# Optimization experiments

Measured on AMD Instinct MI355X. Metric: run time of the kernel, lower is better.

## Reference

```python
import jax, jax.numpy as jnp
import numpy as np

IN_F, HID, OUT, NN = 64, 128, 64, 128
TOTAL = 4096  # 32 graphs * 128 nodes


def setup_inputs() -> dict:
    key = jax.random.key(0)
    ks = jax.random.split(key, 8)
    d_in = 1 + 2 * IN_F
    s1 = 1.0 / np.sqrt(d_in)
    s2 = 1.0 / np.sqrt(HID)
    return {
        "feat": jax.random.normal(ks[0], (TOTAL, IN_F), jnp.float32),
        "coordinate": jax.random.normal(ks[1], (TOTAL, 3), jnp.float32),
        "W1": jax.random.uniform(ks[2], (d_in, HID), jnp.float32, -s1, s1),
        "b1": jax.random.uniform(ks[3], (HID,), jnp.float32, -s1, s1),
        "W2": jax.random.uniform(ks[4], (HID, HID), jnp.float32, -s2, s2),
        "b2": jax.random.uniform(ks[5], (HID,), jnp.float32, -s2, s2),
        "W3": jax.random.uniform(ks[6], (HID, OUT), jnp.float32, -s2, s2),
        "b3": jax.random.uniform(ks[7], (OUT,), jnp.float32, -s2, s2),
        "num_nodes": NN,
    }


def reference(feat, coordinate, W1, b1, W2, b2, W3, b3, num_nodes):
    N = num_nodes
    B = feat.shape[0] // N
    h = feat.reshape(B, N, -1)        # [B,N,F]
    x = coordinate.reshape(B, N, -1)  # [B,N,3]
    # pairwise squared distance: [B,N,N,1]
    d2 = jnp.sum((x[:, None, :, :] - x[:, :, None, :]) ** 2, axis=-1, keepdims=True)
    F = h.shape[-1]
    # feat concat order matches torch: [h_j broadcast over dim1, h_i broadcast over dim2]
    hj = jnp.broadcast_to(h[:, None, :, :], (B, N, N, F))
    hi = jnp.broadcast_to(h[:, :, None, :], (B, N, N, F))
    z = jnp.concatenate([d2, hj, hi], axis=-1)  # [B,N,N,1+2F]
    z = jax.nn.silu(z @ W1 + b1)
    z = jax.nn.silu(z @ W2 + b2)
    z = z @ W3 + b3                   # [B,N,N,OUT]
    return jnp.sum(z, axis=(1, 2))    # [B,OUT]
```

## Files before the change

### kernel.cpp

```cpp
#include <hip/hip_runtime.h>
#include <hip/hip_bf16.h>

#define F_IN 64
#define HID 128
#define OUTF 64
#define NN 128
#define NB 32
#define TOTAL 4096

typedef short bf16x8 __attribute__((ext_vector_type(8)));
typedef float f32x4 __attribute__((ext_vector_type(4)));

static __device__ __forceinline__ short f2bf(float v) {
  __hip_bfloat16 h = __float2bfloat16(v);
  return __builtin_bit_cast(short, h);
}
static __device__ __forceinline__ float fast_silu(float v) {
  return v * __builtin_amdgcn_rcpf(1.f + __expf(-v));
}

__global__ __launch_bounds__(256) void uv_prep(
    const float* __restrict__ feat,
    const float* __restrict__ W1,
    const float* __restrict__ W2,
    const float* __restrict__ b1,
    float* __restrict__ uv,
    __hip_bfloat16* __restrict__ w2swz) {
  __shared__ __align__(16) char wcat[256 * 128];
  const int tid = threadIdx.x;

  {
    const int c = tid;
    const int cc = c & 127;
    const int rbase = (c < HID) ? 1 : 65;
#pragma unroll
    for (int p = 0; p < 8; ++p) {
      bf16x8 pk;
#pragma unroll
      for (int m = 0; m < 8; ++m)
        pk[m] = f2bf(W1[(rbase + p * 8 + m) * HID + cc]);
      *reinterpret_cast<bf16x8*>(wcat + c * 128 + ((p ^ (c & 7)) << 4)) = pk;
    }
  }
  if (blockIdx.x < 64) {
    const int e = blockIdx.x * 256 + tid;
    const int kk = e >> 7, cc2 = e & 127;
    const int byo = cc2 * 256 + (((kk >> 3) ^ (cc2 & 7)) << 4) + (kk & 7) * 2;
    *reinterpret_cast<__hip_bfloat16*>(reinterpret_cast<char*>(w2swz) + byo) =
        __float2bfloat16(W2[kk * HID + cc2]);
  }
  __syncthreads();

  const int wave = tid >> 6, lane = tid & 63;
  const int lr = lane & 15, kg = lane >> 4;
  const int r0 = blockIdx.x * 16;

  f32x4 acc[4];
#pragma unroll
  for (int ct = 0; ct < 4; ++ct) acc[ct] = {0.f, 0.f, 0.f, 0.f};

#pragma unroll
  for (int ks = 0; ks < 2; ++ks) {
    const float* fp = feat + (size_t)(r0 + lr) * F_IN + ks * 32 + kg * 8;
    const f32x4 fa = *reinterpret_cast<const f32x4*>(fp);
    const f32x4 fb = *reinterpret_cast<const f32x4*>(fp + 4);
    bf16x8 a;
#pragma unroll
    for (int m = 0; m < 4; ++m) {
      a[m] = f2bf(fa[m]);
      a[4 + m] = f2bf(fb[m]);
    }
    const int slot = ks * 4 + kg;
#pragma unroll
    for (int ct = 0; ct < 4; ++ct) {
      const int c = wave * 64 + ct * 16 + lr;
      const bf16x8 w = *reinterpret_cast<const bf16x8*>(
          wcat + c * 128 + ((slot ^ (c & 7)) << 4));
      acc[ct] = __builtin_amdgcn_mfma_f32_16x16x32_bf16(a, w, acc[ct], 0, 0, 0);
    }
  }
#pragma unroll
  for (int ct = 0; ct < 4; ++ct) {
    const int c = wave * 64 + ct * 16 + lr;
    const float badd = (c >= HID) ? b1[c - HID] : 0.f;
#pragma unroll
    for (int reg = 0; reg < 4; ++reg) {
      const int r = r0 + kg * 4 + reg;
      uv[(size_t)r * 256 + c] = acc[ct][reg] + badd;
    }
  }
}

__global__ __launch_bounds__(512) void sake_main(
    const float* __restrict__ coord,
    const float* __restrict__ W1,
    const float* __restrict__ b2,
    const float* __restrict__ uv,
    const __hip_bfloat16* __restrict__ w2swz,
    float* __restrict__ part) {
  __shared__ __align__(16) char w2lds[HID * 256];
  __shared__ float ssum[8][HID];

  const int tid = threadIdx.x;
  const int bid = (blockIdx.x & 7) * 512 + (blockIdx.x >> 3);
  const int b = bid >> 7;
  const int i = bid & 127;

#pragma unroll
  for (int p = 0; p < 4; ++p) {
    const int o = (tid + p * 512) * 16;
    *reinterpret_cast<int4*>(w2lds + o) =
        *reinterpret_cast<const int4*>(reinterpret_cast<const char*>(w2swz) + o);
  }

  const int wave = tid >> 6, lane = tid & 63;
  const int lr = lane & 15, kg = lane >> 4;
  const int j = wave * 16 + lr;

  const float* xj = coord + (size_t)(b * NN + j) * 3;
  const float* xi = coord + (size_t)(b * NN + i) * 3;
  const float dx = xj[0] - xi[0], dy = xj[1] - xi[1], dz = xj[2] - xi[2];
  const float d2j = dx * dx + dy * dy + dz * dz;

  f32x4 acc[8];
#pragma unroll
  for (int ct = 0; ct < 8; ++ct) {
    const float bb = b2[ct * 16 + lr];
    acc[ct] = {bb, bb, bb, bb};
  }

  const float* urow = uv + (size_t)(b * NN + j) * 256;
  const float* vrow = uv + (size_t)(b * NN + i) * 256 + HID;

  __syncthreads();

#pragma unroll
  for (int ks = 0; ks < 4; ++ks) {
    const int c0 = ks * 32 + kg * 8;
    const f32x4 ua = *reinterpret_cast<const f32x4*>(urow + c0);
    const f32x4 ub = *reinterpret_cast<const f32x4*>(urow + c0 + 4);
    const f32x4 va = *reinterpret_cast<const f32x4*>(vrow + c0);
    const f32x4 vb = *reinterpret_cast<const f32x4*>(vrow + c0 + 4);
    const f32x4 wa = *reinterpret_cast<const f32x4*>(W1 + c0);
    const f32x4 wb = *reinterpret_cast<const f32x4*>(W1 + c0 + 4);
    bf16x8 a;
#pragma unroll
    for (int m = 0; m < 4; ++m) {
      a[m] = f2bf(fast_silu(fmaf(d2j, wa[m], ua[m] + va[m])));
      a[4 + m] = f2bf(fast_silu(fmaf(d2j, wb[m], ub[m] + vb[m])));
    }
    const int slot = ks * 4 + kg;
    const int rbase = lr * 256 + ((slot ^ (lr & 7)) << 4);
#pragma unroll
    for (int ct = 0; ct < 8; ++ct) {
      const bf16x8 w = *reinterpret_cast<const bf16x8*>(w2lds + rbase + ct * 4096);
      acc[ct] = __builtin_amdgcn_mfma_f32_16x16x32_bf16(a, w, acc[ct], 0, 0, 0);
    }
  }

  float csum[8];
#pragma unroll
  for (int ct = 0; ct < 8; ++ct) {
    float s = fast_silu(acc[ct][0]) + fast_silu(acc[ct][1]) +
              fast_silu(acc[ct][2]) + fast_silu(acc[ct][3]);
    s += __shfl_xor(s, 16);
    s += __shfl_xor(s, 32);
    csum[ct] = s;
  }
  if (lane < 16) {
#pragma unroll
    for (int ct = 0; ct < 8; ++ct) ssum[wave][ct * 16 + lane] = csum[ct];
  }
  __syncthreads();
  if (tid < HID) {
    float s = 0.f;
#pragma unroll
    for (int w = 0; w < 8; ++w) s += ssum[w][tid];
    part[(size_t)bid * HID + tid] = s;
  }
}

__global__ void final_kernel(const float* __restrict__ part,
                             const float* __restrict__ W3,
                             const float* __restrict__ b3,
                             float* __restrict__ out) {
  __shared__ float s2[2][HID];
  __shared__ float s[HID];
  int b = blockIdx.x, t = threadIdx.x;
  int c = t & 127, half = t >> 7;
  float a = 0.f;
  for (int i = half * 64; i < half * 64 + 64; ++i)
    a += part[(size_t)(b * NN + i) * HID + c];
  s2[half][c] = a;
  __syncthreads();
  if (t < HID) s[t] = s2[0][t] + s2[1][t];
  __syncthreads();
  if (t < OUTF) {
    float o = 16384.f * b3[t];
    for (int c2 = 0; c2 < HID; ++c2) o += s[c2] * W3[c2 * OUTF + t];
    out[b * OUTF + t] = o;
  }
}

extern "C" void kernel_launch(void* const* d_in, const int* in_sizes, int n_in,
                              void* d_out, int out_size, void* d_ws, size_t ws_size,
                              hipStream_t stream) {
  const float* feat = (const float*)d_in[0];
  const float* coord = (const float*)d_in[1];
  const float* W1 = (const float*)d_in[2];
  const float* b1 = (const float*)d_in[3];
  const float* W2 = (const float*)d_in[4];
  const float* b2 = (const float*)d_in[5];
  const float* W3 = (const float*)d_in[6];
  const float* b3 = (const float*)d_in[7];
  float* out = (float*)d_out;

  char* ws = (char*)d_ws;
  __hip_bfloat16* w2swz = (__hip_bfloat16*)ws;
  float* uv = (float*)(ws + 64 * 1024);
  float* part = (float*)(ws + 64 * 1024 + 4096 * 1024);

  uv_prep<<<256, 256, 0, stream>>>(feat, W1, W2, b1, uv, w2swz);
  sake_main<<<TOTAL, 512, 0, stream>>>(coord, W1, b2, uv, w2swz, part);
  final_kernel<<<NB, 256, 0, stream>>>(part, W3, b3, out);
}
```

Measured before the change: 70.54 us.

## Process four i-rows per block and reuse W2 fragments across j-tiles

Each block of sake_main now handles four i nodes instead of one, with two waves per i each covering 64 j columns as four 16-row tiles. W2 fragments are loaded from LDS once per k-step into registers and reused across the four tiles. The per-block W2 LDS fill is also amortised over four times more work, since the grid drops from 4096 to 1024 blocks. The cost is a 32-entry accumulator array per thread, which raises register pressure, and launch bounds now request two blocks per CU. The final reduction kernel is adjusted to match the new partial-sum layout.

```diff
diff --git a/kernel.cpp b/kernel.cpp
--- a/kernel.cpp
+++ b/kernel.cpp
@@ -91,7 +91,7 @@
   }
 }
 
-__global__ __launch_bounds__(512) void sake_main(
+__global__ __launch_bounds__(512, 2) void sake_main(
     const float* __restrict__ coord,
     const float* __restrict__ W1,
     const float* __restrict__ b2,
@@ -102,9 +102,9 @@
   __shared__ float ssum[8][HID];
 
   const int tid = threadIdx.x;
-  const int bid = (blockIdx.x & 7) * 512 + (blockIdx.x >> 3);
-  const int b = bid >> 7;
-  const int i = bid & 127;
+  const int bid = (blockIdx.x & 7) * 128 + (blockIdx.x >> 3);
+  const int b = bid >> 5;
+  const int ig = bid & 31;
 
 #pragma unroll
   for (int p = 0; p < 4; ++p) {
@@ -115,54 +115,75 @@
 
   const int wave = tid >> 6, lane = tid & 63;
   const int lr = lane & 15, kg = lane >> 4;
-  const int j = wave * 16 + lr;
-
-  const float* xj = coord + (size_t)(b * NN + j) * 3;
+  const int i = ig * 4 + (wave >> 1);
+  const int j0 = (wave & 1) * 64;
+
   const float* xi = coord + (size_t)(b * NN + i) * 3;
-  const float dx = xj[0] - xi[0], dy = xj[1] - xi[1], dz = xj[2] - xi[2];
-  const float d2j = dx * dx + dy * dy + dz * dz;
-
-  f32x4 acc[8];
+  const float xix = xi[0], xiy = xi[1], xiz = xi[2];
+  float d2t[4];
+#pragma unroll
+  for (int t = 0; t < 4; ++t) {
+    const float* xj = coord + (size_t)(b * NN + j0 + t * 16 + lr) * 3;
+    const float dx = xj[0] - xix, dy = xj[1] - xiy, dz = xj[2] - xiz;
+    d2t[t] = dx * dx + dy * dy + dz * dz;
+  }
+
+  f32x4 acc[4][8];
 #pragma unroll
   for (int ct = 0; ct < 8; ++ct) {
     const float bb = b2[ct * 16 + lr];
-    acc[ct] = {bb, bb, bb, bb};
-  }
-
-  const float* urow = uv + (size_t)(b * NN + j) * 256;
-  const float* vrow = uv + (size_t)(b * NN + i) * 256 + HID;
+#pragma unroll
+    for (int t = 0; t < 4; ++t) acc[t][ct] = {bb, bb, bb, bb};
+  }
+
+  const float* vrow = uv + ((size_t)b * NN + i) * 256 + HID;
+  const float* urow0 = uv + ((size_t)b * NN + j0 + lr) * 256;
 
   __syncthreads();
 
 #pragma unroll
   for (int ks = 0; ks < 4; ++ks) {
     const int c0 = ks * 32 + kg * 8;
-    const f32x4 ua = *reinterpret_cast<const f32x4*>(urow + c0);
-    const f32x4 ub = *reinterpret_cast<const f32x4*>(urow + c0 + 4);
+    bf16x8 wf[8];
+    const int rbase = lr * 256 + ((((ks << 2) | kg) ^ (lr & 7)) << 4);
+#pragma unroll
+    for (int ct = 0; ct < 8; ++ct)
+      wf[ct] = *reinterpret_cast<const bf16x8*>(w2lds + rbase + ct * 4096);
+
     const f32x4 va = *reinterpret_cast<const f32x4*>(vrow + c0);
     const f32x4 vb = *reinterpret_cast<const f32x4*>(vrow + c0 + 4);
     const f32x4 wa = *reinterpret_cast<const f32x4*>(W1 + c0);
     const f32x4 wb = *reinterpret_cast<const f32x4*>(W1 + c0 + 4);
-    bf16x8 a;
-#pragma unroll
-    for (int m = 0; m < 4; ++m) {
-      a[m] = f2bf(fast_silu(fmaf(d2j, wa[m], ua[m] + va[m])));
-      a[4 + m] = f2bf(fast_silu(fmaf(d2j, wb[m], ub[m] + vb[m])));
-    }
-    const int slot = ks * 4 + kg;
-    const int rbase = lr * 256 + ((slot ^ (lr & 7)) << 4);
-#pragma unroll
-    for (int ct = 0; ct < 8; ++ct) {
-      const bf16x8 w = *reinterpret_cast<const bf16x8*>(w2lds + rbase + ct * 4096);
-      acc[ct] = __builtin_amdgcn_mfma_f32_16x16x32_bf16(a, w, acc[ct], 0, 0, 0);
+
+#pragma unroll
+    for (int t = 0; t < 4; ++t) {
+      const float* up = urow0 + t * 4096 + c0;
+      const f32x4 ua = *reinterpret_cast<const f32x4*>(up);
+      const f32x4 ub = *reinterpret_cast<const f32x4*>(up + 4);
+      bf16x8 a;
+#pragma unroll
+      for (int m = 0; m < 4; ++m) {
+        a[m] = f2bf(fast_silu(fmaf(d2t[t], wa[m], ua[m] + va[m])));
+        a[4 + m] = f2bf(fast_silu(fmaf(d2t[t], wb[m], ub[m] + vb[m])));
+      }
+#pragma unroll
+      for (int ct = 0; ct < 8; ++ct)
+        acc[t][ct] = __builtin_amdgcn_mfma_f32_16x16x32_bf16(a, wf[ct],
+                                                             acc[t][ct], 0, 0, 0);
     }
   }
 
   float csum[8];
 #pragma unroll
   for (int ct = 0; ct < 8; ++ct) {
-    float s = fast_silu(acc[ct][0]) + fast_silu(acc[ct][1]) +
-              fast_silu(acc[ct][2]) + fast_silu(acc[ct][3]);
+    float s = 0.f;
+#pragma unroll
+    for (int t = 0; t < 4; ++t)
+#pragma unroll
+      for (int reg = 0; reg < 4; ++reg) {
+        const float v = acc[t][ct][reg];
+        s = fmaf(v, __builtin_amdgcn_rcpf(1.f + __expf(-v)), s);
+      }
     s += __shfl_xor(s, 16);
     s += __shfl_xor(s, 32);
     csum[ct] = s;
@@ -189,8 +210,8 @@
   int b = blockIdx.x, t = threadIdx.x;
   int c = t & 127, half = t >> 7;
   float a = 0.f;
-  for (int i = half * 64; i < half * 64 + 64; ++i)
-    a += part[(size_t)(b * NN + i) * HID + c];
+  for (int g = half * 16; g < half * 16 + 16; ++g)
+    a += part[(size_t)(b * 32 + g) * HID + c];
   s2[half][c] = a;
   __syncthreads();
   if (t < HID) s[t] = s2[0][t] + s2[1][t];
@@ -221,6 +242,6 @@
   float* part = (float*)(ws + 64 * 1024 + 4096 * 1024);
 
   uv_prep<<<256, 256, 0, stream>>>(feat, W1, W2, b1, uv, w2swz);
-  sake_main<<<TOTAL, 512, 0, stream>>>(coord, W1, b2, uv, w2swz, part);
+  sake_main<<<1024, 512, 0, stream>>>(coord, W1, b2, uv, w2swz, part);
   final_kernel<<<NB, 256, 0, stream>>>(part, W3, b3, out);
 }
```

Result: faster. 68.82 us (-2.4%).

## Hold W2 in registers, one wave per node i, prescale SiLU by -log2e

Applied to the files above, without the earlier changes.

The main kernel is restructured so each wave handles one target node i and loops over j in chunks of 16. Half of the transposed W2 stays in registers for the whole loop and the other half is reloaded from global memory on each chunk, which removes the shared-memory staging and the block-wide sync. The weights, biases and u/v are prescaled by -log2(e) so SiLU uses a raw exp2 without extra multiplies, and final_kernel undoes the scale with -ln2. Register pressure rises and the per-chunk W2 reloads depend on cache hits; the swapped MFMA operand order also changes the reduction layout to a 16-lane shuffle.

```diff
diff --git a/kernel.cpp b/kernel.cpp
--- a/kernel.cpp
+++ b/kernel.cpp
@@ -8,6 +8,9 @@
 #define NB 32
 #define TOTAL 4096
 
+#define NEG_LOG2E (-1.4426950408889634f)
+#define NEG_LN2 (-0.6931471805599453f)
+
 typedef short bf16x8 __attribute__((ext_vector_type(8)));
 typedef float f32x4 __attribute__((ext_vector_type(4)));
 
@@ -15,8 +18,13 @@
   __hip_bfloat16 h = __float2bfloat16(v);
   return __builtin_bit_cast(short, h);
 }
-static __device__ __forceinline__ float fast_silu(float v) {
-  return v * __builtin_amdgcn_rcpf(1.f + __expf(-v));
+
+static __device__ __forceinline__ float fexp2(float x) {
+#if __has_builtin(__builtin_amdgcn_exp2f)
+  return __builtin_amdgcn_exp2f(x);
+#else
+  return exp2f(x);
+#endif
 }
 
 __global__ __launch_bounds__(256) void uv_prep(
@@ -24,11 +32,13 @@
     const float* __restrict__ W1,
     const float* __restrict__ W2,
     const float* __restrict__ b1,
-    float* __restrict__ uv,
-    __hip_bfloat16* __restrict__ w2swz) {
+    const float* __restrict__ b2,
+    float* __restrict__ uvp,
+    __hip_bfloat16* __restrict__ w2t,
+    float* __restrict__ w0p,
+    float* __restrict__ b2p) {
   __shared__ __align__(16) char wcat[256 * 128];
   const int tid = threadIdx.x;
-
   {
     const int c = tid;
     const int cc = c & 127;
@@ -45,9 +55,10 @@
   if (blockIdx.x < 64) {
     const int e = blockIdx.x * 256 + tid;
     const int kk = e >> 7, cc2 = e & 127;
-    const int byo = cc2 * 256 + (((kk >> 3) ^ (cc2 & 7)) << 4) + (kk & 7) * 2;
-    *reinterpret_cast<__hip_bfloat16*>(reinterpret_cast<char*>(w2swz) + byo) =
-        __float2bfloat16(W2[kk * HID + cc2]);
+    w2t[cc2 * HID + kk] = __float2bfloat16(W2[kk * HID + cc2]);
+  } else if (blockIdx.x == 64) {
+    if (tid < HID) w0p[tid] = NEG_LOG2E * W1[tid];
+    else b2p[tid - HID] = NEG_LOG2E * b2[tid - HID];
   }
   __syncthreads();
 
@@ -86,97 +97,128 @@
 #pragma unroll
     for (int reg = 0; reg < 4; ++reg) {
       const int r = r0 + kg * 4 + reg;
-      uv[(size_t)r * 256 + c] = acc[ct][reg] + badd;
-    }
-  }
-}
-
-__global__ __launch_bounds__(512) void sake_main(
+      uvp[(size_t)r * 256 + c] = NEG_LOG2E * (acc[ct][reg] + badd);
+    }
+  }
+}
+
+__global__ __launch_bounds__(256, 2) void sake_main(
     const float* __restrict__ coord,
-    const float* __restrict__ W1,
-    const float* __restrict__ b2,
-    const float* __restrict__ uv,
-    const __hip_bfloat16* __restrict__ w2swz,
+    const float* __restrict__ w0p,
+    const float* __restrict__ b2p,
+    const float* __restrict__ uvp,
+    const __hip_bfloat16* __restrict__ w2t,
     float* __restrict__ part) {
-  __shared__ __align__(16) char w2lds[HID * 256];
-  __shared__ float ssum[8][HID];
-
   const int tid = threadIdx.x;
-  const int bid = (blockIdx.x & 7) * 512 + (blockIdx.x >> 3);
-  const int b = bid >> 7;
-  const int i = bid & 127;
-
-#pragma unroll
-  for (int p = 0; p < 4; ++p) {
-    const int o = (tid + p * 512) * 16;
-    *reinterpret_cast<int4*>(w2lds + o) =
-        *reinterpret_cast<const int4*>(reinterpret_cast<const char*>(w2swz) + o);
-  }
-
   const int wave = tid >> 6, lane = tid & 63;
   const int lr = lane & 15, kg = lane >> 4;
-  const int j = wave * 16 + lr;
-
-  const float* xj = coord + (size_t)(b * NN + j) * 3;
+  const int bid = (blockIdx.x & 7) * 128 + (blockIdx.x >> 3);
+  const int gi = bid * 4 + wave;
+  const int b = gi >> 7, i = gi & 127;
+
+  const short* w2s = reinterpret_cast<const short*>(w2t);
+
+  bf16x8 w2f[4][4];
+#pragma unroll
+  for (int cht = 0; cht < 4; ++cht)
+#pragma unroll
+    for (int ks = 0; ks < 4; ++ks)
+      w2f[cht][ks] = *reinterpret_cast<const bf16x8*>(
+          w2s + (cht * 16 + lr) * HID + ks * 32 + kg * 8);
+
   const float* xi = coord + (size_t)(b * NN + i) * 3;
-  const float dx = xj[0] - xi[0], dy = xj[1] - xi[1], dz = xj[2] - xi[2];
-  const float d2j = dx * dx + dy * dy + dz * dz;
-
-  f32x4 acc[8];
-#pragma unroll
-  for (int ct = 0; ct < 8; ++ct) {
-    const float bb = b2[ct * 16 + lr];
-    acc[ct] = {bb, bb, bb, bb};
-  }
-
-  const float* urow = uv + (size_t)(b * NN + j) * 256;
-  const float* vrow = uv + (size_t)(b * NN + i) * 256 + HID;
-
-  __syncthreads();
-
-#pragma unroll
-  for (int ks = 0; ks < 4; ++ks) {
-    const int c0 = ks * 32 + kg * 8;
-    const f32x4 ua = *reinterpret_cast<const f32x4*>(urow + c0);
-    const f32x4 ub = *reinterpret_cast<const f32x4*>(urow + c0 + 4);
-    const f32x4 va = *reinterpret_cast<const f32x4*>(vrow + c0);
-    const f32x4 vb = *reinterpret_cast<const f32x4*>(vrow + c0 + 4);
-    const f32x4 wa = *reinterpret_cast<const f32x4*>(W1 + c0);
-    const f32x4 wb = *reinterpret_cast<const f32x4*>(W1 + c0 + 4);
-    bf16x8 a;
+  const float xix = xi[0], xiy = xi[1], xiz = xi[2];
+  const float* vrow = uvp + ((size_t)b * NN + i) * 256 + HID;
+  const float* ubase = uvp + (size_t)b * NN * 256;
+
+  f32x4 csum[8];
+#pragma unroll
+  for (int c = 0; c < 8; ++c) csum[c] = {0.f, 0.f, 0.f, 0.f};
+
+#pragma unroll 2
+  for (int ch = 0; ch < 8; ++ch) {
+    const int j = ch * 16 + lr;
+
+    bf16x8 wl[4][4];
+#pragma unroll
+    for (int c4 = 0; c4 < 4; ++c4)
+#pragma unroll
+      for (int ks = 0; ks < 4; ++ks)
+        wl[c4][ks] = *reinterpret_cast<const bf16x8*>(
+            w2s + ((4 + c4) * 16 + lr) * HID + ks * 32 + kg * 8);
+
+    const float* xj = coord + (size_t)(b * NN + j) * 3;
+    const float dx = xj[0] - xix, dy = xj[1] - xiy, dz = xj[2] - xiz;
+    const float d2 = dx * dx + dy * dy + dz * dz;
+
+    const float* urow = ubase + (size_t)j * 256;
+    bf16x8 zb[4];
+#pragma unroll
+    for (int ks = 0; ks < 4; ++ks) {
+      const int c0 = ks * 32 + kg * 8;
+      const f32x4 ua = *reinterpret_cast<const f32x4*>(urow + c0);
+      const f32x4 ub = *reinterpret_cast<const f32x4*>(urow + c0 + 4);
+      const f32x4 va = *reinterpret_cast<const f32x4*>(vrow + c0);
+      const f32x4 vb = *reinterpret_cast<const f32x4*>(vrow + c0 + 4);
+      const f32x4 wa = *reinterpret_cast<const f32x4*>(w0p + c0);
+      const f32x4 wb = *reinterpret_cast<const f32x4*>(w0p + c0 + 4);
+#pragma unroll
+      for (int m = 0; m < 4; ++m) {
+        const float z = fmaf(d2, wa[m], ua[m] + va[m]);
+        const float s = z * __builtin_amdgcn_rcpf(1.f + fexp2(z));
+        zb[ks][m] = f2bf(s);
+      }
+#pragma unroll
+      for (int m = 0; m < 4; ++m) {
+        const float z = fmaf(d2, wb[m], ub[m] + vb[m]);
+        const float s = z * __builtin_amdgcn_rcpf(1.f + fexp2(z));
+        zb[ks][4 + m] = f2bf(s);
+      }
+    }
+
+    f32x4 acc[8];
+#pragma unroll
+    for (int c = 0; c < 8; ++c)
+      acc[c] = *reinterpret_cast<const f32x4*>(b2p + c * 16 + kg * 4);
+
+#pragma unroll
+    for (int ks = 0; ks < 4; ++ks) {
+#pragma unroll
+      for (int c = 0; c < 4; ++c)
+        acc[c] = __builtin_amdgcn_mfma_f32_16x16x32_bf16(w2f[c][ks], zb[ks],
+                                                         acc[c], 0, 0, 0);
+#pragma unroll
+      for (int c = 0; c < 4; ++c)
+        acc[4 + c] = __builtin_amdgcn_mfma_f32_16x16x32_bf16(wl[c][ks], zb[ks],
+                                                             acc[4 + c], 0, 0, 0);
+    }
+
+#pragma unroll
+    for (int c = 0; c < 8; ++c)
+#pragma unroll
+      for (int m = 0; m < 4; ++m) {
+        const float z = acc[c][m];
+        const float y = __builtin_amdgcn_rcpf(1.f + fexp2(z));
+        csum[c][m] = fmaf(z, y, csum[c][m]);
+      }
+  }
+
+#pragma unroll
+  for (int c = 0; c < 8; ++c)
 #pragma unroll
     for (int m = 0; m < 4; ++m) {
-      a[m] = f2bf(fast_silu(fmaf(d2j, wa[m], ua[m] + va[m])));
-      a[4 + m] = f2bf(fast_silu(fmaf(d2j, wb[m], ub[m] + vb[m])));
-    }
-    const int slot = ks * 4 + kg;
-    const int rbase = lr * 256 + ((slot ^ (lr & 7)) << 4);
-#pragma unroll
-    for (int ct = 0; ct < 8; ++ct) {
-      const bf16x8 w = *reinterpret_cast<const bf16x8*>(w2lds + rbase + ct * 4096);
-      acc[ct] = __builtin_amdgcn_mfma_f32_16x16x32_bf16(a, w, acc[ct], 0, 0, 0);
-    }
-  }
-
-  float csum[8];
-#pragma unroll
-  for (int ct = 0; ct < 8; ++ct) {
-    float s = fast_silu(acc[ct][0]) + fast_silu(acc[ct][1]) +
-              fast_silu(acc[ct][2]) + fast_silu(acc[ct][3]);
-    s += __shfl_xor(s, 16);
-    s += __shfl_xor(s, 32);
-    csum[ct] = s;
-  }
-  if (lane < 16) {
-#pragma unroll
-    for (int ct = 0; ct < 8; ++ct) ssum[wave][ct * 16 + lane] = csum[ct];
-  }
-  __syncthreads();
-  if (tid < HID) {
-    float s = 0.f;
-#pragma unroll
-    for (int w = 0; w < 8; ++w) s += ssum[w][tid];
-    part[(size_t)bid * HID + tid] = s;
+      float s = csum[c][m];
+      s += __shfl_xor(s, 1);
+      s += __shfl_xor(s, 2);
+      s += __shfl_xor(s, 4);
+      s += __shfl_xor(s, 8);
+      csum[c][m] = s;
+    }
+  if (lr == 0) {
+    float* dst = part + (size_t)gi * HID;
+#pragma unroll
+    for (int c = 0; c < 8; ++c)
+      *reinterpret_cast<f32x4*>(dst + c * 16 + kg * 4) = csum[c];
   }
 }
 
@@ -189,11 +231,11 @@
   int b = blockIdx.x, t = threadIdx.x;
   int c = t & 127, half = t >> 7;
   float a = 0.f;
-  for (int i = half * 64; i < half * 64 + 64; ++i)
-    a += part[(size_t)(b * NN + i) * HID + c];
+  for (int g = half * 64; g < half * 64 + 64; ++g)
+    a += part[(size_t)(b * NN + g) * HID + c];
   s2[half][c] = a;
   __syncthreads();
-  if (t < HID) s[t] = s2[0][t] + s2[1][t];
+  if (t < HID) s[t] = (s2[0][t] + s2[1][t]) * NEG_LN2;
   __syncthreads();
   if (t < OUTF) {
     float o = 16384.f * b3[t];
@@ -216,11 +258,13 @@
   float* out = (float*)d_out;
 
   char* ws = (char*)d_ws;
-  __hip_bfloat16* w2swz = (__hip_bfloat16*)ws;
-  float* uv = (float*)(ws + 64 * 1024);
+  __hip_bfloat16* w2t = (__hip_bfloat16*)ws;
+  float* w0p = (float*)(ws + 32 * 1024);
+  float* b2p = (float*)(ws + 36 * 1024);
+  float* uvp = (float*)(ws + 64 * 1024);
   float* part = (float*)(ws + 64 * 1024 + 4096 * 1024);
 
-  uv_prep<<<256, 256, 0, stream>>>(feat, W1, W2, b1, uv, w2swz);
-  sake_main<<<TOTAL, 512, 0, stream>>>(coord, W1, b2, uv, w2swz, part);
+  uv_prep<<<256, 256, 0, stream>>>(feat, W1, W2, b1, b2, uvp, w2t, w0p, b2p);
+  sake_main<<<1024, 256, 0, stream>>>(coord, w0p, b2p, uvp, w2t, part);
   final_kernel<<<NB, 256, 0, stream>>>(part, W3, b3, out);
 }
```

Result: slower. 193.3 us (+174.1%).
